# Performance work log

Measured on AMD Instinct MI355X. Metric: run time of the kernel, lower is better.

## Reference

```python
import jax, jax.numpy as jnp
import numpy as np
import math

K_HISTORY = 32  # sliding-window length over GRU hidden states


def rotate_half(x):
    half = x.shape[-1] // 2
    return jnp.concatenate([-x[..., half:], x[..., :half]], axis=-1)


def setup_inputs() -> dict:
    key = jax.random.key(0)
    ks = jax.random.split(key, 8)
    B, MB, IN = 8, 512, 1024          # batch, max_bin, input_size (gru_hidden_size)
    EMB, H, KVH, HD, BS = 1024, 16, 4, 64, 16  # embed_dim, heads, kv_heads, head_dim, bin_size
    h = jax.random.normal(ks[0], (B, MB, IN), jnp.float32)
    # RoPE tables: rotate-half layout, theta repeated over both halves
    pos = jnp.arange(MB, dtype=jnp.float32)
    inv_freq = 1.0 / (10000.0 ** (jnp.arange(0, HD, 2, dtype=jnp.float32) / HD))
    theta = pos[:, None] * inv_freq[None, :]            # (MB, HD/2)
    theta = jnp.concatenate([theta, theta], axis=-1)    # (MB, HD)
    freqs_cos = jnp.cos(theta)
    freqs_sin = jnp.sin(theta)
    s = 0.02
    Wq = jax.random.normal(ks[1], (EMB, H * HD), jnp.float32) * s
    Wk = jax.random.normal(ks[2], (IN, KVH * HD), jnp.float32) * s
    Wv = jax.random.normal(ks[3], (IN, KVH * HD), jnp.float32) * s
    Wo = jax.random.normal(ks[4], (H * HD, EMB), jnp.float32) * s
    output_queries = jax.random.normal(ks[5], (BS, EMB), jnp.float32)
    Wr = jax.random.normal(ks[6], (EMB, 2), jnp.float32) * s
    br = jnp.zeros((2,), jnp.float32)
    return {"h": h, "freqs_cos": freqs_cos, "freqs_sin": freqs_sin,
            "Wq": Wq, "Wk": Wk, "Wv": Wv, "Wo": Wo,
            "output_queries": output_queries, "Wr": Wr, "br": br}


def reference(h, freqs_cos, freqs_sin, Wq, Wk, Wv, Wo, output_queries, Wr, br):
    B, MB, IN = h.shape
    HD = freqs_cos.shape[1]
    H = Wq.shape[1] // HD
    KVH = Wk.shape[1] // HD
    n_rep = H // KVH
    BS = output_queries.shape[0]
    K = K_HISTORY

    # sliding windows over bins: window t covers h[t-K+1 : t+1] (zero left-pad)
    h_padded = jnp.concatenate([jnp.zeros((B, K - 1, IN), h.dtype), h], axis=1)
    idx = jnp.arange(MB)[:, None] + jnp.arange(K)[None, :]   # (MB, K)
    h_win = h_padded[:, idx, :]                              # (B, MB, K, IN)

    k = (h_win @ Wk).reshape(B, MB, K, KVH, HD)
    v = (h_win @ Wv).reshape(B, MB, K, KVH, HD)

    # queries: shared learned output queries, identical across batch & bins
    q = (output_queries @ Wq).reshape(BS, H, HD)             # (BS, H, HD)
    # RoPE on Q only (is_decoder=True) at within-bin offsets 0..BS-1
    offs = jnp.arange(BS)
    cos = freqs_cos[offs][:, None, :]                        # (BS, 1, HD)
    sin = freqs_sin[offs][:, None, :]
    q = q * cos + rotate_half(q) * sin                       # (BS, H, HD)

    # GQA: repeat_interleave KV heads to H heads
    k = jnp.repeat(k, n_rep, axis=3)                         # (B, MB, K, H, HD)
    v = jnp.repeat(v, n_rep, axis=3)

    scores = jnp.einsum("qhd,bmkhd->bmhqk", q, k) / math.sqrt(HD)
    attn = jax.nn.softmax(scores, axis=-1)                   # (B, MB, H, BS, K)
    attn_out = jnp.einsum("bmhqk,bmkhd->bmqhd", attn, v)
    attn_out = attn_out.reshape(B, MB, BS, H * HD)

    z = attn_out @ Wo                                        # (B, MB, BS, EMB)
    vel = z @ Wr + br                                        # (B, MB, BS, 2)
    return vel.reshape(B, MB * BS, 2)
```

## Files before the change

### kernel.cpp

```cpp
#include <hip/hip_runtime.h>


typedef __attribute__((ext_vector_type(8))) short v8s;
typedef __attribute__((ext_vector_type(4))) float v4f;

#define OFF_WOR  0u
#define OFF_QR   2048u
#define OFF_WTH  18432u
#define OFF_WTL  182272u
#define OFF_S0   346112u
#define OFF_S1   1460224u
#define OFF_VW0  2574336u
#define OFF_VW1  2713600u
#define OFF_AH   2852864u
#define OFF_AL   4950016u
#define SROW 544

__device__ __forceinline__ void split_bf16(float a, unsigned short& h, unsigned short& l) {
    const unsigned u = __float_as_uint(a);
    h = (unsigned short)(u >> 16);
    const float r = a - __uint_as_float(u & 0xFFFF0000u);
    unsigned v = __float_as_uint(r);
    v += 0x7FFFu + ((v >> 16) & 1u);
    l = (unsigned short)(v >> 16);
}

__global__ __launch_bounds__(256) void kP(
    const float* __restrict__ oq, const float* __restrict__ Wq,
    const float* __restrict__ fc, const float* __restrict__ fs,
    const float* __restrict__ Wo, const float* __restrict__ Wr,
    const float* __restrict__ hsrc,
    float* __restrict__ qr, float* __restrict__ Wor,
    float* __restrict__ S0, float* __restrict__ S1,
    float* __restrict__ VW0, float* __restrict__ VW1,
    unsigned* __restrict__ wthu, unsigned* __restrict__ wtlu,
    unsigned short* __restrict__ Ahg, unsigned short* __restrict__ Alg)
{
    __shared__ float sm[2048];
    const int b = blockIdx.x, t = threadIdx.x;
    if (b >= 658) {
        const int base = (b - 658) * 2048 + t * 8;
        const float4 x0 = *(const float4*)(hsrc + base);
        const float4 x1 = *(const float4*)(hsrc + base + 4);
        const float af[8] = {x0.x, x0.y, x0.z, x0.w, x1.x, x1.y, x1.z, x1.w};
        v8s ah, al;
        #pragma unroll
        for (int j = 0; j < 8; ++j) {
            unsigned short hh, ll;
            split_bf16(af[j], hh, ll);
            ah[j] = (short)hh; al[j] = (short)ll;
        }
        *(v8s*)(Ahg + base) = ah;
        *(v8s*)(Alg + base) = al;
        return;
    }
    if (b < 256) {
        const int q = b >> 4, h = b & 15;
        #pragma unroll
        for (int j = 0; j < 4; ++j) sm[t + 256 * j] = oq[q * 1024 + t + 256 * j];
        __syncthreads();
        const int w = t >> 6, lane = t & 63;
        const float* wq = Wq + (size_t)(w * 256) * 1024 + h * 64 + lane;
        const float* os = sm + w * 256;
        float acc = 0.f;
        #pragma unroll 16
        for (int e = 0; e < 256; ++e) acc = fmaf(os[e], wq[(size_t)e * 1024], acc);
        sm[1024 + w * 64 + lane] = acc;
        __syncthreads();
        if (t < 64) {
            const int d = t, p = d ^ 32;
            const float a1 = sm[1024 + d] + sm[1088 + d] + sm[1152 + d] + sm[1216 + d];
            const float a2 = sm[1024 + p] + sm[1088 + p] + sm[1152 + p] + sm[1216 + p];
            const float c = fc[q * 64 + d], s = fs[q * 64 + d];
            const float rh = (d < 32) ? -a2 : a2;
            qr[q * 1024 + h * 64 + d] = fmaf(a1, c, rh * s);
        }
    } else if (b < 512) {
        #pragma unroll
        for (int j = 0; j < 8; ++j) sm[t + 256 * j] = Wr[t + 256 * j];
        __syncthreads();
        const int i = (b - 256) * 4 + (t >> 6);
        const int lane = t & 63;
        float a0 = 0.f, a1 = 0.f;
        const float* wo = Wo + (size_t)i * 1024 + lane;
        #pragma unroll
        for (int j = 0; j < 16; ++j) {
            const float w = wo[j * 64];
            const int e = lane + j * 64;
            a0 = fmaf(w, sm[2 * e], a0);
            a1 = fmaf(w, sm[2 * e + 1], a1);
        }
        #pragma unroll
        for (int w = 1; w < 64; w <<= 1) {
            a0 += __shfl_xor(a0, w, 64);
            a1 += __shfl_xor(a1, w, 64);
        }
        if (lane == 0) { Wor[i * 2] = a0; Wor[i * 2 + 1] = a1; }
    } else if (b < 656) {
        const int idx = (b - 512) * 256 + t;
        const float4 z = make_float4(0.f, 0.f, 0.f, 0.f);
        if (idx < 16384)       *(float4*)(S0  + (size_t)(idx >> 3) * SROW + (idx & 7) * 4) = z;
        else if (idx < 32768)  *(float4*)(S1  + (size_t)((idx - 16384) >> 3) * SROW + (idx & 7) * 4) = z;
        else if (idx < 34816)  *(float4*)(VW0 + (size_t)((idx - 32768) >> 3) * SROW + (idx & 7) * 4) = z;
        else                   *(float4*)(VW1 + (size_t)((idx - 34816) >> 3) * SROW + (idx & 7) * 4) = z;
    } else {
        unsigned* dst = (b == 656) ? wthu : wtlu;
        #pragma unroll
        for (int j = 0; j < 64; ++j) dst[147456 + t + 256 * j] = 0u;
    }
}

__global__ __launch_bounds__(256) void kW(
    const float* __restrict__ Wk, const float* __restrict__ Wv,
    const float* __restrict__ qr, const float* __restrict__ Wor,
    unsigned short* __restrict__ Wth, unsigned short* __restrict__ Wtl)
{
    __shared__ float As[16 * 68];
    __shared__ float Bt[72 * 68];
    const int b = blockIdx.x, t = threadIdx.x;
    const int g = b & 3, i0 = (b >> 2) * 16;
    #pragma unroll
    for (int jj = 0; jj < 16; ++jj) {
        const int i2 = t + 256 * jj;
        const int d = i2 & 63, col = i2 >> 6;
        Bt[col * 68 + d] = qr[(col >> 2) * 1024 + (g * 4 + (col & 3)) * 64 + d];
    }
    #pragma unroll
    for (int jj = 0; jj < 2; ++jj) {
        const int i2 = t + 256 * jj;
        const int d = i2 & 63, vc = i2 >> 6;
        Bt[(64 + vc) * 68 + d] = Wor[((g * 4 + (vc >> 1)) * 64 + d) * 2 + (vc & 1)];
    }
    {
        const int i = t >> 4, dc = (t & 15) * 4;
        *(float4*)&As[i * 68 + dc] = *(const float4*)(Wk + (size_t)(i0 + i) * 256 + g * 64 + dc);
    }
    __syncthreads();
    const int jc = t & 63, iq = t >> 6;
    {
        float o4[4] = {0.f, 0.f, 0.f, 0.f};
        #pragma unroll
        for (int dc = 0; dc < 16; ++dc) {
            const float4 bv = *(const float4*)&Bt[jc * 68 + dc * 4];
            #pragma unroll
            for (int r = 0; r < 4; ++r) {
                const float4 av = *(const float4*)&As[(iq * 4 + r) * 68 + dc * 4];
                o4[r] = fmaf(av.x, bv.x, o4[r]);
                o4[r] = fmaf(av.y, bv.y, o4[r]);
                o4[r] = fmaf(av.z, bv.z, o4[r]);
                o4[r] = fmaf(av.w, bv.w, o4[r]);
            }
        }
        const int j = (jc >> 2) * 16 + g * 4 + (jc & 3);
        #pragma unroll
        for (int r = 0; r < 4; ++r) {
            unsigned short hh, ll;
            split_bf16(o4[r] * 0.125f, hh, ll);
            Wth[(size_t)j * 1024 + i0 + iq * 4 + r] = hh;
            Wtl[(size_t)j * 1024 + i0 + iq * 4 + r] = ll;
        }
    }
    __syncthreads();
    {
        const int i = t >> 4, dc = (t & 15) * 4;
        *(float4*)&As[i * 68 + dc] = *(const float4*)(Wv + (size_t)(i0 + i) * 256 + g * 64 + dc);
    }
    __syncthreads();
    if (t < 128) {
        const int il = t >> 3, vc = t & 7;
        float acc = 0.f;
        #pragma unroll
        for (int dc = 0; dc < 16; ++dc) {
            const float4 av = *(const float4*)&As[il * 68 + dc * 4];
            const float4 bv = *(const float4*)&Bt[(64 + vc) * 68 + dc * 4];
            acc = fmaf(av.x, bv.x, acc);
            acc = fmaf(av.y, bv.y, acc);
            acc = fmaf(av.z, bv.z, acc);
            acc = fmaf(av.w, bv.w, acc);
        }
        const int j = 256 + (g * 4 + (vc >> 1)) * 2 + (vc & 1);
        unsigned short hh, ll;
        split_bf16(acc, hh, ll);
        Wth[(size_t)j * 1024 + i0 + il] = hh;
        Wtl[(size_t)j * 1024 + i0 + il] = ll;
    }
}

__global__ __launch_bounds__(256) void k2(
    const unsigned short* __restrict__ Ahg, const unsigned short* __restrict__ Alg,
    const unsigned short* __restrict__ Wth, const unsigned short* __restrict__ Wtl,
    float* __restrict__ S0, float* __restrict__ S1,
    float* __restrict__ VW0, float* __restrict__ VW1)
{
    __shared__ unsigned short Ah[64 * 72], Al[64 * 72];
    __shared__ unsigned short Bh[64 * 72], Bl[64 * 72];
    const int m0 = blockIdx.x * 64;
    const int n0 = blockIdx.y * 64;
    const int kh = blockIdx.z;
    const int t = threadIdx.x;
    const int lane = t & 63, wv = t >> 6;
    const int l16 = lane & 15, quad = lane >> 4;
    const int wm = wv >> 1, wn = wv & 1;
    const int sr = t >> 2, kc = (t & 3) * 8;
    v4f acc[2][2];
    #pragma unroll
    for (int i = 0; i < 2; ++i)
        #pragma unroll
        for (int j = 0; j < 2; ++j) acc[i][j] = (v4f)(0.f);
    const unsigned short* Aph = Ahg + (size_t)(m0 + sr) * 1024 + kh * 512 + kc;
    const unsigned short* Apl = Alg + (size_t)(m0 + sr) * 1024 + kh * 512 + kc;
    const unsigned short* Bph = Wth + (size_t)(n0 + sr) * 1024 + kh * 512 + kc;
    const unsigned short* Bpl = Wtl + (size_t)(n0 + sr) * 1024 + kh * 512 + kc;
    v8s rah0 = *(const v8s*)(Aph);      v8s rah1 = *(const v8s*)(Aph + 32);
    v8s ral0 = *(const v8s*)(Apl);      v8s ral1 = *(const v8s*)(Apl + 32);
    v8s rbh0 = *(const v8s*)(Bph);      v8s rbh1 = *(const v8s*)(Bph + 32);
    v8s rbl0 = *(const v8s*)(Bpl);      v8s rbl1 = *(const v8s*)(Bpl + 32);
    for (int k0 = 0; k0 < 512; k0 += 64) {
        __syncthreads();
        *(v8s*)&Ah[sr * 72 + kc] = rah0;  *(v8s*)&Ah[sr * 72 + kc + 32] = rah1;
        *(v8s*)&Al[sr * 72 + kc] = ral0;  *(v8s*)&Al[sr * 72 + kc + 32] = ral1;
        *(v8s*)&Bh[sr * 72 + kc] = rbh0;  *(v8s*)&Bh[sr * 72 + kc + 32] = rbh1;
        *(v8s*)&Bl[sr * 72 + kc] = rbl0;  *(v8s*)&Bl[sr * 72 + kc + 32] = rbl1;
        __syncthreads();
        if (k0 + 64 < 512) {
            const int kn = k0 + 64;
            rah0 = *(const v8s*)(Aph + kn);  rah1 = *(const v8s*)(Aph + kn + 32);
            ral0 = *(const v8s*)(Apl + kn);  ral1 = *(const v8s*)(Apl + kn + 32);
            rbh0 = *(const v8s*)(Bph + kn);  rbh1 = *(const v8s*)(Bph + kn + 32);
            rbl0 = *(const v8s*)(Bpl + kn);  rbl1 = *(const v8s*)(Bpl + kn + 32);
        }
        #pragma unroll
        for (int kk = 0; kk < 2; ++kk) {
            v8s fah[2], fal[2], fbh[2], fbl[2];
            #pragma unroll
            for (int s = 0; s < 2; ++s) {
                const int mr = wm * 32 + s * 16 + l16;
                fah[s] = *(const v8s*)&Ah[mr * 72 + kk * 32 + quad * 8];
                fal[s] = *(const v8s*)&Al[mr * 72 + kk * 32 + quad * 8];
                const int nr = wn * 32 + s * 16 + l16;
                fbh[s] = *(const v8s*)&Bh[nr * 72 + kk * 32 + quad * 8];
                fbl[s] = *(const v8s*)&Bl[nr * 72 + kk * 32 + quad * 8];
            }
            #pragma unroll
            for (int ms = 0; ms < 2; ++ms)
                #pragma unroll
                for (int ns = 0; ns < 2; ++ns) {
                    acc[ms][ns] = __builtin_amdgcn_mfma_f32_16x16x32_bf16(fal[ms], fbh[ns], acc[ms][ns], 0, 0, 0);
                    acc[ms][ns] = __builtin_amdgcn_mfma_f32_16x16x32_bf16(fah[ms], fbl[ns], acc[ms][ns], 0, 0, 0);
                    acc[ms][ns] = __builtin_amdgcn_mfma_f32_16x16x32_bf16(fah[ms], fbh[ns], acc[ms][ns], 0, 0, 0);
                }
        }
    }
    float* Sh  = kh ? S1 : S0;
    float* VWh = kh ? VW1 : VW0;
    #pragma unroll
    for (int ms = 0; ms < 2; ++ms)
        #pragma unroll
        for (int ns = 0; ns < 2; ++ns) {
            const int j = n0 + wn * 32 + ns * 16 + l16;
            if (j >= 288) continue;
            const int m = m0 + wm * 32 + ms * 16 + quad * 4;
            const int bb = m >> 9, tt = m & 511;
            const float4 v = make_float4(acc[ms][ns][0], acc[ms][ns][1], acc[ms][ns][2], acc[ms][ns][3]);
            float* dst;
            if (j < 256)
                dst = Sh + (size_t)((bb * 16 + (j >> 4)) * 16 + (j & 15)) * SROW + 32 + tt;
            else
                dst = VWh + (size_t)(bb * 32 + (j - 256)) * SROW + 32 + tt;
            *(float4*)dst = v;
        }
}

__global__ __launch_bounds__(256) void k3(
    const float* __restrict__ S0, const float* __restrict__ S1,
    const float* __restrict__ VW0, const float* __restrict__ VW1,
    const float* __restrict__ brp, float* __restrict__ out)
{
    __shared__ float Es[16 * 164];
    __shared__ float EVs[32 * 164];
    const int b = blockIdx.x, q = blockIdx.y, qt = blockIdx.z;
    const int tbase = qt * 128;
    const int t = threadIdx.x;
    for (int idx = t; idx < 640; idx += 256) {
        const int h = idx / 40, g = idx - h * 40;
        const size_t off = (size_t)((b * 16 + q) * 16 + h) * SROW + tbase + g * 4;
        const float4 a = *(const float4*)(S0 + off);
        const float4 c = *(const float4*)(S1 + off);
        float4 e;
        e.x = __expf(a.x + c.x); e.y = __expf(a.y + c.y);
        e.z = __expf(a.z + c.z); e.w = __expf(a.w + c.w);
        *(float4*)(Es + h * 164 + g * 4) = e;
    }
    __syncthreads();
    for (int idx = t; idx < 1280; idx += 256) {
        const int hc = idx / 40, g = idx - hc * 40;
        const size_t off = (size_t)(b * 32 + hc) * SROW + tbase + g * 4;
        const float4 v0 = *(const float4*)(VW0 + off);
        const float4 v1 = *(const float4*)(VW1 + off);
        const float4 e = *(const float4*)(Es + (hc >> 1) * 164 + g * 4);
        float4 rr;
        rr.x = e.x * (v0.x + v1.x); rr.y = e.y * (v0.y + v1.y);
        rr.z = e.z * (v0.z + v1.z); rr.w = e.w * (v0.w + v1.w);
        *(float4*)(EVs + hc * 164 + g * 4) = rr;
    }
    __syncthreads();
    const int h = t & 15, mg = t >> 4;
    const float* ep = Es + h * 164 + mg * 8;
    const float* e0 = EVs + (2 * h) * 164 + mg * 8;
    const float* e1 = EVs + (2 * h + 1) * 164 + mg * 8;
    float den = 0.f, n0s = 0.f, n1s = 0.f;
    #pragma unroll
    for (int s = 0; s < 32; ++s) {
        const int ss = 1 + ((s + 2 * h) & 31);
        den += ep[ss]; n0s += e0[ss]; n1s += e1[ss];
    }
    const float br0 = brp[0], br1 = brp[1];
    #pragma unroll
    for (int u = 0; u < 8; ++u) {
        const float inv = __builtin_amdgcn_rcpf(den);
        float c0 = n0s * inv, c1 = n1s * inv;
        #pragma unroll
        for (int w = 1; w < 16; w <<= 1) {
            c0 += __shfl_xor(c0, w, 64);
            c1 += __shfl_xor(c1, w, 64);
        }
        if (h == 0) {
            const int m = tbase + mg * 8 + u;
            float* o = out + (size_t)((b * 512 + m) * 16 + q) * 2;
            o[0] = c0 + br0;
            o[1] = c1 + br1;
        }
        if (u < 7) {
            den += ep[33 + u] - ep[1 + u];
            n0s += e0[33 + u] - e0[1 + u];
            n1s += e1[33 + u] - e1[1 + u];
        }
    }
}

extern "C" void kernel_launch(void* const* d_in, const int* in_sizes, int n_in,
                              void* d_out, int out_size, void* d_ws, size_t ws_size,
                              hipStream_t stream)
{
    (void)in_sizes; (void)n_in; (void)out_size; (void)ws_size;
    const float* h  = (const float*)d_in[0];
    const float* fc = (const float*)d_in[1];
    const float* fs = (const float*)d_in[2];
    const float* Wq = (const float*)d_in[3];
    const float* Wk = (const float*)d_in[4];
    const float* Wv = (const float*)d_in[5];
    const float* Wo = (const float*)d_in[6];
    const float* oq = (const float*)d_in[7];
    const float* Wr = (const float*)d_in[8];
    const float* br = (const float*)d_in[9];
    float* ws = (float*)d_ws;
    float* Wor  = ws + OFF_WOR;
    float* qr   = ws + OFF_QR;
    unsigned short* Wth = (unsigned short*)(ws + OFF_WTH);
    unsigned short* Wtl = (unsigned short*)(ws + OFF_WTL);
    float* S0   = ws + OFF_S0;
    float* S1   = ws + OFF_S1;
    float* VW0  = ws + OFF_VW0;
    float* VW1  = ws + OFF_VW1;
    unsigned short* Ahg = (unsigned short*)(ws + OFF_AH);
    unsigned short* Alg = (unsigned short*)(ws + OFF_AL);
    float* out = (float*)d_out;

    hipLaunchKernelGGL(kP, dim3(2706), dim3(256), 0, stream,
                       oq, Wq, fc, fs, Wo, Wr, h, qr, Wor, S0, S1, VW0, VW1,
                       (unsigned*)Wth, (unsigned*)Wtl, Ahg, Alg);
    hipLaunchKernelGGL(kW, dim3(256), dim3(256), 0, stream, Wk, Wv, qr, Wor, Wth, Wtl);
    hipLaunchKernelGGL(k2, dim3(64, 5, 2), dim3(256), 0, stream, Ahg, Alg, Wth, Wtl, S0, S1, VW0, VW1);
    hipLaunchKernelGGL(k3, dim3(8, 16, 4), dim3(256), 0, stream, S0, S1, VW0, VW1, br, out);
}
```

Before: 122.3 us.

## Load A fragments directly from global in k2 and use 2-wave blocks

The k2 split-bf16 GEMM no longer stages the A operand through shared memory. Each wave loads its A MFMA fragments straight from global memory, and only B is staged in LDS. The block shrinks from 4 waves to 2, with each wave covering 32 rows by 64 columns, which doubles its per-wave accumulators. This cuts LDS traffic and shared-memory footprint, at the cost of uncoalesced A loads issued without prefetch ahead of the barrier, fewer threads per block and higher register pressure.

```diff
diff --git a/kernel.cpp b/kernel.cpp
--- a/kernel.cpp
+++ b/kernel.cpp
@@ -186,82 +186,96 @@
     }
 }
 
-__global__ __launch_bounds__(256) void k2(
+__global__ __launch_bounds__(128) void k2(
     const unsigned short* __restrict__ Ahg, const unsigned short* __restrict__ Alg,
     const unsigned short* __restrict__ Wth, const unsigned short* __restrict__ Wtl,
     float* __restrict__ S0, float* __restrict__ S1,
     float* __restrict__ VW0, float* __restrict__ VW1)
 {
-    __shared__ unsigned short Ah[64 * 72], Al[64 * 72];
     __shared__ unsigned short Bh[64 * 72], Bl[64 * 72];
     const int m0 = blockIdx.x * 64;
     const int n0 = blockIdx.y * 64;
     const int kh = blockIdx.z;
     const int t = threadIdx.x;
-    const int lane = t & 63, wv = t >> 6;
+    const int lane = t & 63, wm = t >> 6;
     const int l16 = lane & 15, quad = lane >> 4;
-    const int wm = wv >> 1, wn = wv & 1;
-    const int sr = t >> 2, kc = (t & 3) * 8;
-    v4f acc[2][2];
-    #pragma unroll
-    for (int i = 0; i < 2; ++i)
-        #pragma unroll
-        for (int j = 0; j < 2; ++j) acc[i][j] = (v4f)(0.f);
-    const unsigned short* Aph = Ahg + (size_t)(m0 + sr) * 1024 + kh * 512 + kc;
-    const unsigned short* Apl = Alg + (size_t)(m0 + sr) * 1024 + kh * 512 + kc;
-    const unsigned short* Bph = Wth + (size_t)(n0 + sr) * 1024 + kh * 512 + kc;
-    const unsigned short* Bpl = Wtl + (size_t)(n0 + sr) * 1024 + kh * 512 + kc;
-    v8s rah0 = *(const v8s*)(Aph);      v8s rah1 = *(const v8s*)(Aph + 32);
-    v8s ral0 = *(const v8s*)(Apl);      v8s ral1 = *(const v8s*)(Apl + 32);
-    v8s rbh0 = *(const v8s*)(Bph);      v8s rbh1 = *(const v8s*)(Bph + 32);
-    v8s rbl0 = *(const v8s*)(Bpl);      v8s rbl1 = *(const v8s*)(Bpl + 32);
+    v4f acc[2][4];
+    #pragma unroll
+    for (int s = 0; s < 2; ++s)
+        #pragma unroll
+        for (int ns = 0; ns < 4; ++ns) acc[s][ns] = (v4f)(0.f);
+    const unsigned short* ApH[2];
+    const unsigned short* ApL[2];
+    #pragma unroll
+    for (int s = 0; s < 2; ++s) {
+        const size_t off = (size_t)(m0 + wm * 32 + s * 16 + l16) * 1024 + kh * 512 + quad * 8;
+        ApH[s] = Ahg + off;
+        ApL[s] = Alg + off;
+    }
+    int brow[4], bkv[4];
+    #pragma unroll
+    for (int j = 0; j < 4; ++j) { const int idx = t * 4 + j; brow[j] = idx >> 3; bkv[j] = idx & 7; }
+    v8s rbh[4], rbl[4];
+    #pragma unroll
+    for (int j = 0; j < 4; ++j) {
+        const size_t g = (size_t)(n0 + brow[j]) * 1024 + kh * 512 + bkv[j] * 8;
+        rbh[j] = *(const v8s*)(Wth + g);
+        rbl[j] = *(const v8s*)(Wtl + g);
+    }
     for (int k0 = 0; k0 < 512; k0 += 64) {
-        __syncthreads();
-        *(v8s*)&Ah[sr * 72 + kc] = rah0;  *(v8s*)&Ah[sr * 72 + kc + 32] = rah1;
-        *(v8s*)&Al[sr * 72 + kc] = ral0;  *(v8s*)&Al[sr * 72 + kc + 32] = ral1;
-        *(v8s*)&Bh[sr * 72 + kc] = rbh0;  *(v8s*)&Bh[sr * 72 + kc + 32] = rbh1;
-        *(v8s*)&Bl[sr * 72 + kc] = rbl0;  *(v8s*)&Bl[sr * 72 + kc + 32] = rbl1;
+        v8s fah[2][2], fal[2][2];
+        #pragma unroll
+        for (int kk = 0; kk < 2; ++kk)
+            #pragma unroll
+            for (int s = 0; s < 2; ++s) {
+                fah[kk][s] = *(const v8s*)(ApH[s] + k0 + kk * 32);
+                fal[kk][s] = *(const v8s*)(ApL[s] + k0 + kk * 32);
+            }
+        __syncthreads();
+        #pragma unroll
+        for (int j = 0; j < 4; ++j) {
+            *(v8s*)&Bh[brow[j] * 72 + bkv[j] * 8] = rbh[j];
+            *(v8s*)&Bl[brow[j] * 72 + bkv[j] * 8] = rbl[j];
+        }
         __syncthreads();
         if (k0 + 64 < 512) {
-            const int kn = k0 + 64;
-            rah0 = *(const v8s*)(Aph + kn);  rah1 = *(const v8s*)(Aph + kn + 32);
-            ral0 = *(const v8s*)(Apl + kn);  ral1 = *(const v8s*)(Apl + kn + 32);
-            rbh0 = *(const v8s*)(Bph + kn);  rbh1 = *(const v8s*)(Bph + kn + 32);
-            rbl0 = *(const v8s*)(Bpl + kn);  rbl1 = *(const v8s*)(Bpl + kn + 32);
+            #pragma unroll
+            for (int j = 0; j < 4; ++j) {
+                const size_t g = (size_t)(n0 + brow[j]) * 1024 + kh * 512 + (k0 + 64) + bkv[j] * 8;
+                rbh[j] = *(const v8s*)(Wth + g);
+                rbl[j] = *(const v8s*)(Wtl + g);
+            }
         }
         #pragma unroll
         for (int kk = 0; kk < 2; ++kk) {
-            v8s fah[2], fal[2], fbh[2], fbl[2];
-            #pragma unroll
-            for (int s = 0; s < 2; ++s) {
-                const int mr = wm * 32 + s * 16 + l16;
-                fah[s] = *(const v8s*)&Ah[mr * 72 + kk * 32 + quad * 8];
-                fal[s] = *(const v8s*)&Al[mr * 72 + kk * 32 + quad * 8];
-                const int nr = wn * 32 + s * 16 + l16;
-                fbh[s] = *(const v8s*)&Bh[nr * 72 + kk * 32 + quad * 8];
-                fbl[s] = *(const v8s*)&Bl[nr * 72 + kk * 32 + quad * 8];
+            v8s fbh[4], fbl[4];
+            #pragma unroll
+            for (int ns = 0; ns < 4; ++ns) {
+                const int a = (ns * 16 + l16) * 72 + kk * 32 + quad * 8;
+                fbh[ns] = *(const v8s*)&Bh[a];
+                fbl[ns] = *(const v8s*)&Bl[a];
             }
             #pragma unroll
-            for (int ms = 0; ms < 2; ++ms)
+            for (int s = 0; s < 2; ++s)
                 #pragma unroll
-                for (int ns = 0; ns < 2; ++ns) {
-                    acc[ms][ns] = __builtin_amdgcn_mfma_f32_16x16x32_bf16(fal[ms], fbh[ns], acc[ms][ns], 0, 0, 0);
-                    acc[ms][ns] = __builtin_amdgcn_mfma_f32_16x16x32_bf16(fah[ms], fbl[ns], acc[ms][ns], 0, 0, 0);
-                    acc[ms][ns] = __builtin_amdgcn_mfma_f32_16x16x32_bf16(fah[ms], fbh[ns], acc[ms][ns], 0, 0, 0);
+                for (int ns = 0; ns < 4; ++ns) {
+                    acc[s][ns] = __builtin_amdgcn_mfma_f32_16x16x32_bf16(fal[kk][s], fbh[ns], acc[s][ns], 0, 0, 0);
+                    acc[s][ns] = __builtin_amdgcn_mfma_f32_16x16x32_bf16(fah[kk][s], fbl[ns], acc[s][ns], 0, 0, 0);
+                    acc[s][ns] = __builtin_amdgcn_mfma_f32_16x16x32_bf16(fah[kk][s], fbh[ns], acc[s][ns], 0, 0, 0);
                 }
         }
     }
     float* Sh  = kh ? S1 : S0;
     float* VWh = kh ? VW1 : VW0;
     #pragma unroll
-    for (int ms = 0; ms < 2; ++ms)
-        #pragma unroll
-        for (int ns = 0; ns < 2; ++ns) {
-            const int j = n0 + wn * 32 + ns * 16 + l16;
+    for (int s = 0; s < 2; ++s)
+        #pragma unroll
+        for (int ns = 0; ns < 4; ++ns) {
+            const int j = n0 + ns * 16 + l16;
             if (j >= 288) continue;
-            const int m = m0 + wm * 32 + ms * 16 + quad * 4;
+            const int m = m0 + wm * 32 + s * 16 + quad * 4;
             const int bb = m >> 9, tt = m & 511;
-            const float4 v = make_float4(acc[ms][ns][0], acc[ms][ns][1], acc[ms][ns][2], acc[ms][ns][3]);
+            const float4 v = make_float4(acc[s][ns][0], acc[s][ns][1], acc[s][ns][2], acc[s][ns][3]);
             float* dst;
             if (j < 256)
                 dst = Sh + (size_t)((bb * 16 + (j >> 4)) * 16 + (j & 15)) * SROW + 32 + tt;
@@ -370,6 +384,6 @@
                        oq, Wq, fc, fs, Wo, Wr, h, qr, Wor, S0, S1, VW0, VW1,
                        (unsigned*)Wth, (unsigned*)Wtl, Ahg, Alg);
     hipLaunchKernelGGL(kW, dim3(256), dim3(256), 0, stream, Wk, Wv, qr, Wor, Wth, Wtl);
-    hipLaunchKernelGGL(k2, dim3(64, 5, 2), dim3(256), 0, stream, Ahg, Alg, Wth, Wtl, S0, S1, VW0, VW1);
+    hipLaunchKernelGGL(k2, dim3(64, 5, 2), dim3(128), 0, stream, Ahg, Alg, Wth, Wtl, S0, S1, VW0, VW1);
     hipLaunchKernelGGL(k3, dim3(8, 16, 4), dim3(256), 0, stream, S0, S1, VW0, VW1, br, out);
 }
```

New measurement: 124.9 us. 1.02x slower.
